# Kernel tuning notes

Hardware: AMD Instinct MI355X
Metric: run time of the kernel (lower is better)

Reference implementation:

```python
import jax, jax.numpy as jnp
import numpy as np

LN_EPS = 1e-5
NEG_INF = -1e30


def setup_inputs() -> dict:
    key = jax.random.key(0)
    ks = jax.random.split(key, 8)
    B, S, D_MODEL, Q_IN = 1, 2048, 1024, 512
    HI, DI = 16, 64            # indexer heads / head_dim
    H, DQK, DV = 8, 64, 64     # MLA heads, qk_head_dim, v_head_dim
    return {
        "x": jax.random.normal(ks[0], (B, S, D_MODEL), jnp.float32),
        "q_input": jax.random.normal(ks[1], (B, S, Q_IN), jnp.float32),
        "q": jax.random.normal(ks[2], (B, S, H, DQK), jnp.float32),
        "k": jax.random.normal(ks[3], (B, S, H, DQK), jnp.float32),
        "v": jax.random.normal(ks[4], (B, S, H, DV), jnp.float32),
        "w_q": jax.random.normal(ks[5], (Q_IN, HI * DI), jnp.float32) * (Q_IN ** -0.5),
        "w_k": jax.random.normal(ks[6], (D_MODEL, DI), jnp.float32) * (D_MODEL ** -0.5),
        "ln_g": jnp.ones((DI,), jnp.float32),
        "ln_b": jnp.zeros((DI,), jnp.float32),
        "w_weights": jax.random.normal(ks[7], (D_MODEL, HI), jnp.float32) * (D_MODEL ** -0.5),
        "top_k": 128,
    }


def _indexer_topk(x, q_input, w_q, w_k, ln_g, ln_b, w_weights, top_k):
    """Lightning indexer: per-head relevance scores -> weighted sum -> causal top-k indices."""
    B, S, _ = x.shape
    HI = w_weights.shape[1]
    DI = w_k.shape[1]
    qi = (q_input @ w_q).reshape(B, S, HI, DI)          # bqhd
    ki = x @ w_k                                         # bkd
    mu = ki.mean(-1, keepdims=True)
    var = ((ki - mu) ** 2).mean(-1, keepdims=True)
    ki = (ki - mu) * jax.lax.rsqrt(var + LN_EPS) * ln_g + ln_b
    # per-head weights; scores*w summed over h == (sum_h w*q) . k  (fused, same math)
    w = (x @ w_weights) * (HI ** -0.5)                   # bqh
    q_eff = jnp.einsum("bqhd,bqh->bqd", qi, w) * (DI ** -0.5)
    scores = jnp.einsum("bqd,bkd->bqk", q_eff, ki)       # [B,S,S]
    pos = jnp.arange(S)
    causal = jnp.where(pos[None, :] <= pos[:, None], 0.0, NEG_INF).astype(scores.dtype)
    scores = scores + causal[None]
    return jax.lax.top_k(scores, top_k)[1]               # [B,S,K]


def reference(x, q_input, q, k, v, w_q, w_k, ln_g, ln_b, w_weights, top_k):
    B, S, H, DQK = q.shape
    DV = v.shape[-1]
    idx = _indexer_topk(x, q_input, w_q, w_k, ln_g, ln_b, w_weights, top_k)  # [B,S,K]

    qh = q.transpose(0, 2, 1, 3)   # [B,H,Sq,D]
    kh = k.transpose(0, 2, 1, 3)   # [B,H,Sk,D]
    vh = v.transpose(0, 2, 1, 3)

    def gather(kv, ix):            # kv [Sk,D], ix [Sq,K] -> [Sq,K,D]
        return kv[ix]

    gather_h = jax.vmap(gather, in_axes=(0, None))       # over heads, shared idx
    gather_bh = jax.vmap(gather_h, in_axes=(0, 0))       # over batch
    k_sel = gather_bh(kh, idx)     # [B,H,Sq,K,D]
    v_sel = gather_bh(vh, idx)     # [B,H,Sq,K,Dv]

    att = jnp.einsum("bhqd,bhqkd->bhqk", qh, k_sel) * (DQK ** -0.5)
    pos = jnp.arange(S)
    valid = idx[:, None, :, :] <= pos[None, None, :, None]   # causal validity of gathered idx
    att = jnp.where(valid, att, NEG_INF)
    p = jax.nn.softmax(att, axis=-1)
    out = jnp.einsum("bhqk,bhqkd->bhqd", p, v_sel)
    return out.transpose(0, 2, 1, 3)   # [B,S,H,Dv]
```

## Files before the change

kernel.cpp:

```cpp
#include <hip/hip_runtime.h>
#include <hip/hip_bf16.h>
#include <hip/hip_fp16.h>
#include <math.h>

#define S 2048
#define DM 1024
#define QIN 512
#define HI 16
#define DI 64
#define NH 8
#define TOPK 128
#define LN_EPS 1e-5f
#define KP 8
#define KVSZ (S * NH * 64)

typedef float f32x4 __attribute__((ext_vector_type(4)));
typedef short s16x8 __attribute__((ext_vector_type(8)));

__device__ __forceinline__ float wave_sum(float v){
#pragma unroll
  for (int o = 32; o; o >>= 1) v += __shfl_xor(v, o);
  return v;
}
__device__ __forceinline__ float wave_max(float v){
#pragma unroll
  for (int o = 32; o; o >>= 1) v = fmaxf(v, __shfl_xor(v, o));
  return v;
}
__device__ __forceinline__ unsigned short f2bf(float x){
  unsigned u = __float_as_uint(x);
  unsigned r = u + 0x7FFFu + ((u >> 16) & 1u);
  return (unsigned short)(r >> 16);
}
__device__ __forceinline__ float bf2f(unsigned short s){
  return __uint_as_float(((unsigned)s) << 16);
}
__device__ __forceinline__ unsigned short f2h(float x){
  return __half_as_ushort(__float2half_rn(x));
}
union UH2 { unsigned int u; __half2 h; };
__device__ __forceinline__ __half2 as_half2(unsigned int u){ UH2 x; x.u = u; return x.h; }

#define MFMA3(ACC, AH, AL, BH, BL) \
  ACC = __builtin_amdgcn_mfma_f32_16x16x32_bf16(AH, BH, ACC, 0, 0, 0); \
  ACC = __builtin_amdgcn_mfma_f32_16x16x32_bf16(AH, BL, ACC, 0, 0, 0); \
  ACC = __builtin_amdgcn_mfma_f32_16x16x32_bf16(AL, BH, ACC, 0, 0, 0);

#define MFMA6(ACC, AH, AM, AL, BH, BM, BL) \
  ACC = __builtin_amdgcn_mfma_f32_16x16x32_bf16(AH, BH, ACC, 0, 0, 0); \
  ACC = __builtin_amdgcn_mfma_f32_16x16x32_bf16(AH, BM, ACC, 0, 0, 0); \
  ACC = __builtin_amdgcn_mfma_f32_16x16x32_bf16(AM, BH, ACC, 0, 0, 0); \
  ACC = __builtin_amdgcn_mfma_f32_16x16x32_bf16(AH, BL, ACC, 0, 0, 0); \
  ACC = __builtin_amdgcn_mfma_f32_16x16x32_bf16(AL, BH, ACC, 0, 0, 0); \
  ACC = __builtin_amdgcn_mfma_f32_16x16x32_bf16(AM, BM, ACC, 0, 0, 0);

__global__ __launch_bounds__(256) void k_f1(const float* __restrict__ x,
                                            const float* __restrict__ wk,
                                            const float* __restrict__ ww,
                                            float* __restrict__ part,
                                            const float* __restrict__ qin,
                                            unsigned short* __restrict__ Ah,
                                            unsigned short* __restrict__ Al,
                                            const float* __restrict__ k,
                                            unsigned short* __restrict__ kh,
                                            const float* __restrict__ v,
                                            unsigned short* __restrict__ vh,
                                            const float* __restrict__ wq,
                                            unsigned short* __restrict__ Bh,
                                            unsigned short* __restrict__ Bl){
  __shared__ float As[32][68];
  __shared__ float Bs[32][84];
  const int bid = blockIdx.x;
  const int t = threadIdx.x;

  if (bid < 256){
    const int kp = bid & 7;
    const int bm = bid >> 3;
    const int m0 = bm * 64;
    const int tm = (t & 15) * 4;
    const int tn = (t >> 4) * 5;
    float acc[4][5];
#pragma unroll
    for (int i = 0; i < 4; i++)
#pragma unroll
      for (int j = 0; j < 5; j++) acc[i][j] = 0.f;

    for (int kb = 0; kb < (DM / KP) / 32; ++kb){
      const int k0 = kp * (DM / KP) + kb * 32;
#pragma unroll
      for (int i = 0; i < 2; i++){
        int u = t + i * 256;
        int m = u >> 3, c4 = u & 7;
        float4 a = *(const float4*)&x[(size_t)(m0 + m) * DM + k0 + c4 * 4];
        As[c4*4+0][m] = a.x; As[c4*4+1][m] = a.y; As[c4*4+2][m] = a.z; As[c4*4+3][m] = a.w;
      }
#pragma unroll
      for (int i = 0; i < 10; i++){
        int u = t + i * 256;
        int kk = u / 80, nn = u % 80;
        float val = (nn < 64) ? wk[(size_t)(k0 + kk) * 64 + nn]
                              : ww[(size_t)(k0 + kk) * 16 + (nn - 64)];
        Bs[kk][nn] = val;
      }
      __syncthreads();
#pragma unroll
      for (int kk = 0; kk < 32; ++kk){
        float4 a = *(const float4*)&As[kk][tm];
        float av[4] = {a.x, a.y, a.z, a.w};
        float bb[5];
#pragma unroll
        for (int j = 0; j < 5; j++) bb[j] = Bs[kk][tn + j];
#pragma unroll
        for (int i = 0; i < 4; i++)
#pragma unroll
          for (int j = 0; j < 5; j++) acc[i][j] = fmaf(av[i], bb[j], acc[i][j]);
      }
      __syncthreads();
    }
    float* dst = part + (size_t)kp * S * 80;
#pragma unroll
    for (int i = 0; i < 4; i++)
#pragma unroll
      for (int j = 0; j < 5; j++)
        dst[(size_t)(m0 + tm + i) * 80 + tn + j] = acc[i][j];
    return;
  }

  if (bid < 256 + 3072){
    const int SEG0 = S * QIN / 4;
    const int SEG1 = KVSZ / 4;
    int id = (bid - 256) * 256 + t;
    if (id < SEG0){
      float4 f = ((const float4*)qin)[id];
      ushort4 h, lo;
      h.x = f2bf(f.x); lo.x = f2bf(f.x - bf2f(h.x));
      h.y = f2bf(f.y); lo.y = f2bf(f.y - bf2f(h.y));
      h.z = f2bf(f.z); lo.z = f2bf(f.z - bf2f(h.z));
      h.w = f2bf(f.w); lo.w = f2bf(f.w - bf2f(h.w));
      ((ushort4*)Ah)[id] = h;
      ((ushort4*)Al)[id] = lo;
    } else if (id < SEG0 + SEG1){
      int j = id - SEG0;
      float4 f = ((const float4*)k)[j];
      ushort4 o;
      o.x = f2h(f.x); o.y = f2h(f.y); o.z = f2h(f.z); o.w = f2h(f.w);
      ((ushort4*)kh)[j] = o;
    } else {
      int j = id - SEG0 - SEG1;
      float4 f = ((const float4*)v)[j];
      ushort4 o;
      o.x = f2h(f.x); o.y = f2h(f.y); o.z = f2h(f.z); o.w = f2h(f.w);
      ((ushort4*)vh)[j] = o;
    }
    return;
  }

  {
    unsigned short (*lh)[33] = (unsigned short(*)[33])&As[0][0];
    unsigned short (*ll)[33] = (unsigned short(*)[33])&Bs[0][0];
    const int b2 = bid - 3328;
    const int k0 = (b2 & 15) * 32;
    const int n0 = (b2 >> 4) * 32;
    const int c = t & 31, r8 = t >> 5;
#pragma unroll
    for (int i = 0; i < 4; ++i){
      int kk = r8 + i * 8;
      float wv = wq[(size_t)(k0 + kk) * 1024 + n0 + c];
      unsigned short h = f2bf(wv);
      lh[c][kk] = h;
      ll[c][kk] = f2bf(wv - bf2f(h));
    }
    __syncthreads();
    const int kk = t & 31, nl = t >> 5;
#pragma unroll
    for (int i = 0; i < 4; ++i){
      int nn = nl + i * 8;
      Bh[(size_t)(n0 + nn) * QIN + k0 + kk] = lh[nn][kk];
      Bl[(size_t)(n0 + nn) * QIN + k0 + kk] = ll[nn][kk];
    }
  }
}

__global__ __launch_bounds__(256) void k_f2(const float* __restrict__ part,
                                            const float* __restrict__ g,
                                            const float* __restrict__ b,
                                            unsigned short* __restrict__ kih,
                                            unsigned short* __restrict__ kim,
                                            unsigned short* __restrict__ kil,
                                            float* __restrict__ wgt,
                                            const unsigned short* __restrict__ Ah,
                                            const unsigned short* __restrict__ Al,
                                            const unsigned short* __restrict__ Bh,
                                            const unsigned short* __restrict__ Bl,
                                            float* __restrict__ qi){
  __shared__ short Ash[64][72];
  __shared__ short Asl[64][72];
  __shared__ short Bsh[64][72];
  __shared__ short Bsl[64][72];
  const int bid = blockIdx.x;
  const int t = threadIdx.x;
  if (bid < 512){
    const int s = bid * 4 + (t >> 6);
    const int l = t & 63;
    float kv = 0.f;
#pragma unroll
    for (int p = 0; p < KP; p++) kv += part[(size_t)p * S * 80 + (size_t)s * 80 + l];
    float wv = 0.f;
    if (l < 16){
#pragma unroll
      for (int p = 0; p < KP; p++) wv += part[(size_t)p * S * 80 + (size_t)s * 80 + 64 + l];
    }
    float mu = wave_sum(kv) * (1.f / 64.f);
    float d  = kv - mu;
    float var = wave_sum(d * d) * (1.f / 64.f);
    float o = d * (1.f / sqrtf(var + LN_EPS)) * g[l] + b[l];
    unsigned short h = f2bf(o);
    float r1 = o - bf2f(h);
    unsigned short m = f2bf(r1);
    kih[(size_t)s * 64 + l] = h;
    kim[(size_t)s * 64 + l] = m;
    kil[(size_t)s * 64 + l] = f2bf(r1 - bf2f(m));
    if (l < 16) wgt[(size_t)s * 16 + l] = wv * 0.25f;
    return;
  }
  const int b2 = bid - 512;
  const int bn = b2 & 15;
  const int bm = b2 >> 4;
  const int w = t >> 6, l = t & 63;
  const int r = l & 15, kg = l >> 4;
  const int m0 = bm * 64 + (w >> 1) * 32;
  const int n0 = bn * 64 + (w & 1) * 32;
  const int mq = (w >> 1) * 32;
  const int nq = (w & 1) * 32;
  const int srow = t >> 3;
  const int scol = (t & 7) * 8;

  f32x4 acc00 = {0,0,0,0}, acc01 = {0,0,0,0}, acc10 = {0,0,0,0}, acc11 = {0,0,0,0};

  for (int kb = 0; kb < QIN / 64; ++kb){
    const int k0 = kb * 64;
#pragma unroll
    for (int i = 0; i < 2; ++i){
      int row = srow + i * 32;
      size_t ga = (size_t)(bm * 64 + row) * QIN + k0 + scol;
      size_t gb = (size_t)(bn * 64 + row) * QIN + k0 + scol;
      *(s16x8*)&Ash[row][scol] = *(const s16x8*)(Ah + ga);
      *(s16x8*)&Asl[row][scol] = *(const s16x8*)(Al + ga);
      *(s16x8*)&Bsh[row][scol] = *(const s16x8*)(Bh + gb);
      *(s16x8*)&Bsl[row][scol] = *(const s16x8*)(Bl + gb);
    }
    __syncthreads();
#pragma unroll
    for (int ks = 0; ks < 2; ++ks){
      const int ko = ks * 32 + kg * 8;
      s16x8 ah0 = *(const s16x8*)&Ash[mq + r][ko];
      s16x8 ah1 = *(const s16x8*)&Ash[mq + 16 + r][ko];
      s16x8 al0 = *(const s16x8*)&Asl[mq + r][ko];
      s16x8 al1 = *(const s16x8*)&Asl[mq + 16 + r][ko];
      s16x8 bh0 = *(const s16x8*)&Bsh[nq + r][ko];
      s16x8 bh1 = *(const s16x8*)&Bsh[nq + 16 + r][ko];
      s16x8 bl0 = *(const s16x8*)&Bsl[nq + r][ko];
      s16x8 bl1 = *(const s16x8*)&Bsl[nq + 16 + r][ko];
      MFMA3(acc00, ah0, al0, bh0, bl0)
      MFMA3(acc01, ah0, al0, bh1, bl1)
      MFMA3(acc10, ah1, al1, bh0, bl0)
      MFMA3(acc11, ah1, al1, bh1, bl1)
    }
    __syncthreads();
  }
#pragma unroll
  for (int j = 0; j < 4; ++j){
    qi[(size_t)(m0 +  0 + kg * 4 + j) * 1024 + n0 +  0 + r] = acc00[j];
    qi[(size_t)(m0 +  0 + kg * 4 + j) * 1024 + n0 + 16 + r] = acc01[j];
    qi[(size_t)(m0 + 16 + kg * 4 + j) * 1024 + n0 +  0 + r] = acc10[j];
    qi[(size_t)(m0 + 16 + kg * 4 + j) * 1024 + n0 + 16 + r] = acc11[j];
  }
}

__global__ __launch_bounds__(256) void k_f3(const float* __restrict__ qi,
                                            const float* __restrict__ wgt,
                                            unsigned short* __restrict__ qeh,
                                            unsigned short* __restrict__ qem,
                                            unsigned short* __restrict__ qel){
  const int id = blockIdx.x * 256 + threadIdx.x;
  const int s = id >> 6, d = id & 63;
  float acc = 0.f;
#pragma unroll
  for (int h = 0; h < 16; h++)
    acc = fmaf(wgt[(size_t)s * 16 + h], qi[(size_t)s * 1024 + h * 64 + d], acc);
  acc *= 0.125f;
  unsigned short hh = f2bf(acc);
  float r1 = acc - bf2f(hh);
  unsigned short mm = f2bf(r1);
  qeh[(size_t)s * 64 + d] = hh;
  qem[(size_t)s * 64 + d] = mm;
  qel[(size_t)s * 64 + d] = f2bf(r1 - bf2f(mm));
}

__global__ __launch_bounds__(256) void k_scores(const unsigned short* __restrict__ qeh,
                                                const unsigned short* __restrict__ qem,
                                                const unsigned short* __restrict__ qel,
                                                const unsigned short* __restrict__ kih,
                                                const unsigned short* __restrict__ kim,
                                                const unsigned short* __restrict__ kil,
                                                float* __restrict__ sc){
  const int bj = blockIdx.x, bi = blockIdx.y;
  if (bj > bi) return;
  const int w = threadIdx.x >> 6, l = threadIdx.x & 63;
  const int r = l & 15, kg = l >> 4;
  const int m0 = bi * 64 + (w >> 1) * 32;
  const int n0 = bj * 64 + (w & 1) * 32;
  f32x4 acc00 = {0,0,0,0}, acc01 = {0,0,0,0}, acc10 = {0,0,0,0}, acc11 = {0,0,0,0};
  const size_t aoff = (size_t)(m0 + r) * 64 + kg * 8;
  const size_t boff = (size_t)(n0 + r) * 64 + kg * 8;
#pragma unroll
  for (int k0 = 0; k0 < 64; k0 += 32){
    s16x8 ah0 = *(const s16x8*)(qeh + aoff + k0);
    s16x8 ah1 = *(const s16x8*)(qeh + aoff + 16 * 64 + k0);
    s16x8 am0 = *(const s16x8*)(qem + aoff + k0);
    s16x8 am1 = *(const s16x8*)(qem + aoff + 16 * 64 + k0);
    s16x8 al0 = *(const s16x8*)(qel + aoff + k0);
    s16x8 al1 = *(const s16x8*)(qel + aoff + 16 * 64 + k0);
    s16x8 bh0 = *(const s16x8*)(kih + boff + k0);
    s16x8 bh1 = *(const s16x8*)(kih + boff + 16 * 64 + k0);
    s16x8 bm0 = *(const s16x8*)(kim + boff + k0);
    s16x8 bm1 = *(const s16x8*)(kim + boff + 16 * 64 + k0);
    s16x8 bl0 = *(const s16x8*)(kil + boff + k0);
    s16x8 bl1 = *(const s16x8*)(kil + boff + 16 * 64 + k0);
    MFMA6(acc00, ah0, am0, al0, bh0, bm0, bl0)
    MFMA6(acc01, ah0, am0, al0, bh1, bm1, bl1)
    MFMA6(acc10, ah1, am1, al1, bh0, bm0, bl0)
    MFMA6(acc11, ah1, am1, al1, bh1, bm1, bl1)
  }
#pragma unroll
  for (int j = 0; j < 4; ++j){
    sc[(size_t)(m0 +  0 + kg * 4 + j) * S + n0 +  0 + r] = acc00[j];
    sc[(size_t)(m0 +  0 + kg * 4 + j) * S + n0 + 16 + r] = acc01[j];
    sc[(size_t)(m0 + 16 + kg * 4 + j) * S + n0 +  0 + r] = acc10[j];
    sc[(size_t)(m0 + 16 + kg * 4 + j) * S + n0 + 16 + r] = acc11[j];
  }
}

__global__ __launch_bounds__(256) void k_topk(const float* __restrict__ sc,
                                              int* __restrict__ idx,
                                              int* __restrict__ cnt){
  const int i = blockIdx.x, t = threadIdx.x;
  const int w = t >> 6, l = t & 63;
  const int n = i + 1;
  int* outr = idx + (size_t)i * TOPK;
  if (n <= TOPK){
    for (int m = t; m < n; m += 256) outr[m] = m;
    if (t == 0) cnt[i] = n;
    return;
  }
  __shared__ unsigned int keys[S];
  __shared__ int lA[S];
  __shared__ int lB[S];
  __shared__ int hist[256];
  __shared__ int wtot[4];
  __shared__ int s_b, s_above, s_out, s_m;
  hist[t] = 0;
  if (t == 0) s_out = 0;
  __syncthreads();
  for (int j = t; j < n; j += 256){
    unsigned int u = __float_as_uint(sc[(size_t)i * S + j]);
    unsigned int kk = (u & 0x80000000u) ? ~u : (u | 0x80000000u);
    keys[j] = kk;
    atomicAdd(&hist[kk >> 24], 1);
  }
  __syncthreads();
  int rem = TOPK;
  {
    const int h = hist[t];
    int vsc = h;
#pragma unroll
    for (int off = 1; off < 64; off <<= 1){
      int u = __shfl_down(vsc, off);
      if (l + off < 64) vsc += u;
    }
    if (l == 0) wtot[w] = vsc;
    __syncthreads();
    int later = 0;
#pragma unroll
    for (int ww = 1; ww < 4; ++ww) if (ww > w) later += wtot[ww];
    const int excl = vsc + later - h;
    if (excl < rem && excl + h >= rem){ s_b = t; s_above = excl; }
    __syncthreads();
  }
  int b = s_b;
  rem -= s_above;
  if (t == 0) s_m = 0;
  __syncthreads();
  for (int j = t; j < n; j += 256){
    int by = keys[j] >> 24;
    if (by > b){ int p = atomicAdd(&s_out, 1); outr[p] = j; }
    else if (by == b){ int p = atomicAdd(&s_m, 1); lA[p] = j; }
  }
  __syncthreads();
  int m = s_m;
  int* Lsrc = lA; int* Ldst = lB;
  bool done = false;
  if (m == rem){
    int base = TOPK - rem;
    for (int u = t; u < m; u += 256) outr[base + u] = Lsrc[u];
    done = true;
  }
  for (int p = 2; p >= 0 && !done; --p){
    const int sh = p * 8;
    __syncthreads();
    hist[t] = 0;
    __syncthreads();
    for (int u = t; u < m; u += 256) atomicAdd(&hist[(keys[Lsrc[u]] >> sh) & 255], 1);
    __syncthreads();
    {
      const int h = hist[t];
      int vsc = h;
#pragma unroll
      for (int off = 1; off < 64; off <<= 1){
        int u = __shfl_down(vsc, off);
        if (l + off < 64) vsc += u;
      }
      if (l == 0) wtot[w] = vsc;
      __syncthreads();
      int later = 0;
#pragma unroll
      for (int ww = 1; ww < 4; ++ww) if (ww > w) later += wtot[ww];
      const int excl = vsc + later - h;
      if (excl < rem && excl + h >= rem){ s_b = t; s_above = excl; }
      __syncthreads();
    }
    b = s_b;
    rem -= s_above;
    if (t == 0) s_m = 0;
    __syncthreads();
    for (int u = t; u < m; u += 256){
      int j = Lsrc[u]; int by = (keys[j] >> sh) & 255;
      if (by > b){ int p2 = atomicAdd(&s_out, 1); outr[p2] = j; }
      else if (by == b){ int p2 = atomicAdd(&s_m, 1); Ldst[p2] = j; }
    }
    __syncthreads();
    m = s_m;
    { int* tmp = Lsrc; Lsrc = Ldst; Ldst = tmp; }
    if (m == rem){
      int base = TOPK - rem;
      for (int u = t; u < m; u += 256) outr[base + u] = Lsrc[u];
      done = true;
    }
  }
  if (!done && t == 0){
    int base = TOPK - rem;
    for (int a = 0; a < rem; ++a){
      int mn = 1 << 30, pos = -1;
      for (int u = 0; u < m; ++u){ int j = Lsrc[u]; if (j < mn){ mn = j; pos = u; } }
      outr[base + a] = mn; Lsrc[pos] = 1 << 30;
    }
  }
  if (t == 0) cnt[i] = TOPK;
}

__global__ __launch_bounds__(256) void k_attn(const float* __restrict__ q,
                                              const unsigned short* __restrict__ kh,
                                              const unsigned short* __restrict__ vh,
                                              const int* __restrict__ idx,
                                              const int* __restrict__ cnt,
                                              float* __restrict__ out){
  const int i = blockIdx.x;
  const int w = threadIdx.x >> 6, l = threadIdx.x & 63;
  const int n = cnt[i];
  const int* irow = idx + (size_t)i * TOPK;

  __shared__ int   sidx[4][TOPK];
  __shared__ float sp[4][2][TOPK];

  sidx[w][l]      = (l < n)      ? irow[l]      : 0;
  sidx[w][l + 64] = (l + 64 < n) ? irow[l + 64] : 0;

  const int h0 = 2 * w, h1 = h0 + 1;
  const int g = l >> 3, gl = l & 7;
  const float* qrow = q + (size_t)i * (NH * 64);
  __half2 qa2[4], qb2[4];
  {
    float4 a0 = *(const float4*)&qrow[h0 * 64 + gl * 8];
    float4 a1 = *(const float4*)&qrow[h0 * 64 + gl * 8 + 4];
    float4 b0 = *(const float4*)&qrow[h1 * 64 + gl * 8];
    float4 b1 = *(const float4*)&qrow[h1 * 64 + gl * 8 + 4];
    qa2[0] = __floats2half2_rn(a0.x * 0.125f, a0.y * 0.125f);
    qa2[1] = __floats2half2_rn(a0.z * 0.125f, a0.w * 0.125f);
    qa2[2] = __floats2half2_rn(a1.x * 0.125f, a1.y * 0.125f);
    qa2[3] = __floats2half2_rn(a1.z * 0.125f, a1.w * 0.125f);
    qb2[0] = __floats2half2_rn(b0.x * 0.125f, b0.y * 0.125f);
    qb2[1] = __floats2half2_rn(b0.z * 0.125f, b0.w * 0.125f);
    qb2[2] = __floats2half2_rn(b1.x * 0.125f, b1.y * 0.125f);
    qb2[3] = __floats2half2_rn(b1.z * 0.125f, b1.w * 0.125f);
  }
  asm volatile("" ::: "memory");

#pragma unroll 4
  for (int pass = 0; pass < TOPK / 8; ++pass){
    const int j = pass * 8 + g;
    const size_t base = (size_t)sidx[w][j] * (NH * 64);
    uint4 u0 = *(const uint4*)(kh + base + h0 * 64 + gl * 8);
    uint4 u1 = *(const uint4*)(kh + base + h1 * 64 + gl * 8);
    __half2 acc0 = __floats2half2_rn(0.f, 0.f);
    __half2 acc1 = __floats2half2_rn(0.f, 0.f);
    acc0 = __hfma2(as_half2(u0.x), qa2[0], acc0);
    acc0 = __hfma2(as_half2(u0.y), qa2[1], acc0);
    acc0 = __hfma2(as_half2(u0.z), qa2[2], acc0);
    acc0 = __hfma2(as_half2(u0.w), qa2[3], acc0);
    acc1 = __hfma2(as_half2(u1.x), qb2[0], acc1);
    acc1 = __hfma2(as_half2(u1.y), qb2[1], acc1);
    acc1 = __hfma2(as_half2(u1.z), qb2[2], acc1);
    acc1 = __hfma2(as_half2(u1.w), qb2[3], acc1);
    float d0 = __low2float(acc0) + __high2float(acc0);
    float d1 = __low2float(acc1) + __high2float(acc1);
#pragma unroll
    for (int o = 1; o < 8; o <<= 1){ d0 += __shfl_xor(d0, o); d1 += __shfl_xor(d1, o); }
    if (gl == 0){ sp[w][0][j] = d0; sp[w][1][j] = d1; }
  }
  asm volatile("" ::: "memory");

  const bool v0 = (l < n), v1 = (l + 64 < n);
  {
    float s0 = v0 ? sp[w][0][l] : -1e30f, s1 = v1 ? sp[w][0][l + 64] : -1e30f;
    float m = wave_max(fmaxf(s0, s1));
    float e0 = v0 ? __expf(s0 - m) : 0.f;
    float e1 = v1 ? __expf(s1 - m) : 0.f;
    float inv = 1.f / wave_sum(e0 + e1);
    sp[w][0][l] = e0 * inv;
    sp[w][0][l + 64] = e1 * inv;
  }
  {
    float s0 = v0 ? sp[w][1][l] : -1e30f, s1 = v1 ? sp[w][1][l + 64] : -1e30f;
    float m = wave_max(fmaxf(s0, s1));
    float e0 = v0 ? __expf(s0 - m) : 0.f;
    float e1 = v1 ? __expf(s1 - m) : 0.f;
    float inv = 1.f / wave_sum(e0 + e1);
    sp[w][1][l] = e0 * inv;
    sp[w][1][l + 64] = e1 * inv;
  }
  asm volatile("" ::: "memory");

  const int kq = l >> 4;
  const int hp = (l >> 3) & 1;
  const int d8 = (l & 7) * 8;
  float o8[8] = {0,0,0,0,0,0,0,0};
#pragma unroll 4
  for (int pass = 0; pass < TOPK / 4; ++pass){
    const int j = pass * 4 + kq;
    const size_t base = (size_t)sidx[w][j] * (NH * 64);
    uint4 uv = *(const uint4*)(vh + base + (h0 + hp) * 64 + d8);
    float p = sp[w][hp][j];
    __half2 va = as_half2(uv.x), vb = as_half2(uv.y), vc = as_half2(uv.z), vd = as_half2(uv.w);
    o8[0] = fmaf(p, __low2float(va),  o8[0]);
    o8[1] = fmaf(p, __high2float(va), o8[1]);
    o8[2] = fmaf(p, __low2float(vb),  o8[2]);
    o8[3] = fmaf(p, __high2float(vb), o8[3]);
    o8[4] = fmaf(p, __low2float(vc),  o8[4]);
    o8[5] = fmaf(p, __high2float(vc), o8[5]);
    o8[6] = fmaf(p, __low2float(vd),  o8[6]);
    o8[7] = fmaf(p, __high2float(vd), o8[7]);
  }
#pragma unroll
  for (int e = 0; e < 8; ++e){
    o8[e] += __shfl_xor(o8[e], 16);
    o8[e] += __shfl_xor(o8[e], 32);
  }
  if (l < 16){
    float* dst = &out[(size_t)i * (NH * 64) + (h0 + hp) * 64 + d8];
    *(float4*)dst       = make_float4(o8[0], o8[1], o8[2], o8[3]);
    *(float4*)(dst + 4) = make_float4(o8[4], o8[5], o8[6], o8[7]);
  }
}

extern "C" void kernel_launch(void* const* d_in, const int* in_sizes, int n_in,
                              void* d_out, int out_size, void* d_ws, size_t ws_size,
                              hipStream_t stream){
  const float* x   = (const float*)d_in[0];
  const float* qin = (const float*)d_in[1];
  const float* q   = (const float*)d_in[2];
  const float* k   = (const float*)d_in[3];
  const float* v   = (const float*)d_in[4];
  const float* wq  = (const float*)d_in[5];
  const float* wk  = (const float*)d_in[6];
  const float* lng = (const float*)d_in[7];
  const float* lnb = (const float*)d_in[8];
  const float* ww  = (const float*)d_in[9];
  float* out = (float*)d_out;

  float* ws = (float*)d_ws;
  float* part = ws;
  float* wgt  = ws + 1310720;
  float* qi   = ws + 1343488;
  float* sc   = ws + 3440640;
  int*   idx  = (int*)(ws + 7634944);
  int*   cnt  = (int*)(ws + 7897088);
  unsigned short* kh  = (unsigned short*)(ws + 7899136);
  unsigned short* vh  = (unsigned short*)(ws + 8423424);
  unsigned short* kih = (unsigned short*)(ws + 8947712);
  unsigned short* kim = (unsigned short*)(ws + 9013248);
  unsigned short* kil = (unsigned short*)(ws + 9078784);
  unsigned short* qeh = (unsigned short*)(ws + 9144320);
  unsigned short* qem = (unsigned short*)(ws + 9209856);
  unsigned short* qel = (unsigned short*)(ws + 9275392);
  unsigned short* Ah  = (unsigned short*)(ws + 9340928);
  unsigned short* Al  = (unsigned short*)(ws + 9865216);
  unsigned short* Bh  = (unsigned short*)(ws + 10389504);
  unsigned short* Bl  = (unsigned short*)(ws + 10651648);

  hipLaunchKernelGGL(k_f1,     dim3(3840),   dim3(256), 0, stream,
                     x, wk, ww, part, qin, Ah, Al, k, kh, v, vh, wq, Bh, Bl);
  hipLaunchKernelGGL(k_f2,     dim3(1024),   dim3(256), 0, stream,
                     part, lng, lnb, kih, kim, kil, wgt, Ah, Al, Bh, Bl, qi);
  hipLaunchKernelGGL(k_f3,     dim3(512),    dim3(256), 0, stream,
                     qi, wgt, qeh, qem, qel);
  hipLaunchKernelGGL(k_scores, dim3(32, 32), dim3(256), 0, stream,
                     qeh, qem, qel, kih, kim, kil, sc);
  hipLaunchKernelGGL(k_topk,   dim3(2048),   dim3(256), 0, stream, sc, idx, cnt);
  hipLaunchKernelGGL(k_attn,   dim3(2048),   dim3(256), 0, stream, q, kh, vh, idx, cnt, out);
}
```

Measured before the change: 97.88 us.

## Fuse top-k selection into sparse attention kernel and double split-K partitions

```diff
diff --git a/kernel.cpp b/kernel.cpp
--- a/kernel.cpp
+++ b/kernel.cpp
@@ -11,7 +11,7 @@
 #define NH 8
 #define TOPK 128
 #define LN_EPS 1e-5f
-#define KP 8
+#define KP 16
 #define KVSZ (S * NH * 64)
 
 typedef float f32x4 __attribute__((ext_vector_type(4)));
@@ -73,9 +73,9 @@
   const int bid = blockIdx.x;
   const int t = threadIdx.x;
 
-  if (bid < 256){
-    const int kp = bid & 7;
-    const int bm = bid >> 3;
+  if (bid < 512){
+    const int kp = bid & 15;
+    const int bm = bid >> 4;
     const int m0 = bm * 64;
     const int tm = (t & 15) * 4;
     const int tn = (t >> 4) * 5;
@@ -126,10 +126,10 @@
     return;
   }
 
-  if (bid < 256 + 3072){
+  if (bid < 512 + 3072){
     const int SEG0 = S * QIN / 4;
     const int SEG1 = KVSZ / 4;
-    int id = (bid - 256) * 256 + t;
+    int id = (bid - 512) * 256 + t;
     if (id < SEG0){
       float4 f = ((const float4*)qin)[id];
       ushort4 h, lo;
@@ -158,7 +158,7 @@
   {
     unsigned short (*lh)[33] = (unsigned short(*)[33])&As[0][0];
     unsigned short (*ll)[33] = (unsigned short(*)[33])&Bs[0][0];
-    const int b2 = bid - 3328;
+    const int b2 = bid - 3584;
     const int k0 = (b2 & 15) * 32;
     const int n0 = (b2 >> 4) * 32;
     const int c = t & 31, r8 = t >> 5;
@@ -341,77 +341,39 @@
   }
 }
 
-__global__ __launch_bounds__(256) void k_topk(const float* __restrict__ sc,
-                                              int* __restrict__ idx,
-                                              int* __restrict__ cnt){
+__global__ __launch_bounds__(256) void k_ta(const float* __restrict__ sc,
+                                            const float* __restrict__ q,
+                                            const unsigned short* __restrict__ kh,
+                                            const unsigned short* __restrict__ vh,
+                                            float* __restrict__ out){
   const int i = blockIdx.x, t = threadIdx.x;
   const int w = t >> 6, l = t & 63;
-  const int n = i + 1;
-  int* outr = idx + (size_t)i * TOPK;
-  if (n <= TOPK){
-    for (int m = t; m < n; m += 256) outr[m] = m;
-    if (t == 0) cnt[i] = n;
-    return;
-  }
+  const int ncand = i + 1;
+
   __shared__ unsigned int keys[S];
   __shared__ int lA[S];
   __shared__ int lB[S];
   __shared__ int hist[256];
   __shared__ int wtot[4];
+  __shared__ int sres[TOPK];
   __shared__ int s_b, s_above, s_out, s_m;
-  hist[t] = 0;
-  if (t == 0) s_out = 0;
-  __syncthreads();
-  for (int j = t; j < n; j += 256){
-    unsigned int u = __float_as_uint(sc[(size_t)i * S + j]);
-    unsigned int kk = (u & 0x80000000u) ? ~u : (u | 0x80000000u);
-    keys[j] = kk;
-    atomicAdd(&hist[kk >> 24], 1);
-  }
-  __syncthreads();
-  int rem = TOPK;
-  {
-    const int h = hist[t];
-    int vsc = h;
-#pragma unroll
-    for (int off = 1; off < 64; off <<= 1){
-      int u = __shfl_down(vsc, off);
-      if (l + off < 64) vsc += u;
-    }
-    if (l == 0) wtot[w] = vsc;
-    __syncthreads();
-    int later = 0;
-#pragma unroll
-    for (int ww = 1; ww < 4; ++ww) if (ww > w) later += wtot[ww];
-    const int excl = vsc + later - h;
-    if (excl < rem && excl + h >= rem){ s_b = t; s_above = excl; }
-    __syncthreads();
-  }
-  int b = s_b;
-  rem -= s_above;
-  if (t == 0) s_m = 0;
-  __syncthreads();
-  for (int j = t; j < n; j += 256){
-    int by = keys[j] >> 24;
-    if (by > b){ int p = atomicAdd(&s_out, 1); outr[p] = j; }
-    else if (by == b){ int p = atomicAdd(&s_m, 1); lA[p] = j; }
-  }
-  __syncthreads();
-  int m = s_m;
-  int* Lsrc = lA; int* Ldst = lB;
-  bool done = false;
-  if (m == rem){
-    int base = TOPK - rem;
-    for (int u = t; u < m; u += 256) outr[base + u] = Lsrc[u];
-    done = true;
-  }
-  for (int p = 2; p >= 0 && !done; --p){
-    const int sh = p * 8;
-    __syncthreads();
+  __shared__ float sp[4][2][TOPK];
+
+  if (ncand <= TOPK){
+    if (t < TOPK) sres[t] = (t < ncand) ? t : 0;
+    __syncthreads();
+  } else {
     hist[t] = 0;
-    __syncthreads();
-    for (int u = t; u < m; u += 256) atomicAdd(&hist[(keys[Lsrc[u]] >> sh) & 255], 1);
-    __syncthreads();
+    if (t == 0) s_out = 0;
+    __syncthreads();
+    for (int j = t; j < ncand; j += 256){
+      unsigned int u = __float_as_uint(sc[(size_t)i * S + j]);
+      unsigned int kk = (u & 0x80000000u) ? ~u : (u | 0x80000000u);
+      keys[j] = kk;
+      atomicAdd(&hist[kk >> 24], 1);
+    }
+    __syncthreads();
+    int rem = TOPK;
     {
       const int h = hist[t];
       int vsc = h;
@@ -429,52 +391,93 @@
       if (excl < rem && excl + h >= rem){ s_b = t; s_above = excl; }
       __syncthreads();
     }
-    b = s_b;
+    int b = s_b;
     rem -= s_above;
     if (t == 0) s_m = 0;
     __syncthreads();
-    for (int u = t; u < m; u += 256){
-      int j = Lsrc[u]; int by = (keys[j] >> sh) & 255;
-      if (by > b){ int p2 = atomicAdd(&s_out, 1); outr[p2] = j; }
-      else if (by == b){ int p2 = atomicAdd(&s_m, 1); Ldst[p2] = j; }
-    }
-    __syncthreads();
-    m = s_m;
-    { int* tmp = Lsrc; Lsrc = Ldst; Ldst = tmp; }
+    for (int b0 = 0; b0 < ncand; b0 += 256){
+      int j = b0 + t;
+      bool valid = j < ncand;
+      unsigned int kk = valid ? keys[j] : 0u;
+      int by = kk >> 24;
+      bool pgt = valid && (by > b);
+      bool peq = valid && (by == b);
+      unsigned long long mgt = __ballot(pgt);
+      unsigned long long meq = __ballot(peq);
+      int basegt = 0, baseeq = 0;
+      if (l == 0){
+        basegt = atomicAdd(&s_out, __popcll(mgt));
+        baseeq = atomicAdd(&s_m, __popcll(meq));
+      }
+      basegt = __shfl(basegt, 0);
+      baseeq = __shfl(baseeq, 0);
+      unsigned long long lanemask = (1ull << l) - 1ull;
+      if (pgt) sres[basegt + __popcll(mgt & lanemask)] = j;
+      if (peq) lA[baseeq + __popcll(meq & lanemask)] = j;
+    }
+    __syncthreads();
+    int m = s_m;
+    int* Lsrc = lA; int* Ldst = lB;
+    bool done = false;
     if (m == rem){
       int base = TOPK - rem;
-      for (int u = t; u < m; u += 256) outr[base + u] = Lsrc[u];
+      for (int u = t; u < m; u += 256) sres[base + u] = Lsrc[u];
       done = true;
     }
-  }
-  if (!done && t == 0){
-    int base = TOPK - rem;
-    for (int a = 0; a < rem; ++a){
-      int mn = 1 << 30, pos = -1;
-      for (int u = 0; u < m; ++u){ int j = Lsrc[u]; if (j < mn){ mn = j; pos = u; } }
-      outr[base + a] = mn; Lsrc[pos] = 1 << 30;
-    }
-  }
-  if (t == 0) cnt[i] = TOPK;
-}
-
-__global__ __launch_bounds__(256) void k_attn(const float* __restrict__ q,
-                                              const unsigned short* __restrict__ kh,
-                                              const unsigned short* __restrict__ vh,
-                                              const int* __restrict__ idx,
-                                              const int* __restrict__ cnt,
-                                              float* __restrict__ out){
-  const int i = blockIdx.x;
-  const int w = threadIdx.x >> 6, l = threadIdx.x & 63;
-  const int n = cnt[i];
-  const int* irow = idx + (size_t)i * TOPK;
-
-  __shared__ int   sidx[4][TOPK];
-  __shared__ float sp[4][2][TOPK];
-
-  sidx[w][l]      = (l < n)      ? irow[l]      : 0;
-  sidx[w][l + 64] = (l + 64 < n) ? irow[l + 64] : 0;
-
+    for (int p = 2; p >= 0 && !done; --p){
+      const int sh = p * 8;
+      __syncthreads();
+      hist[t] = 0;
+      __syncthreads();
+      for (int u = t; u < m; u += 256) atomicAdd(&hist[(keys[Lsrc[u]] >> sh) & 255], 1);
+      __syncthreads();
+      {
+        const int h = hist[t];
+        int vsc = h;
+#pragma unroll
+        for (int off = 1; off < 64; off <<= 1){
+          int u = __shfl_down(vsc, off);
+          if (l + off < 64) vsc += u;
+        }
+        if (l == 0) wtot[w] = vsc;
+        __syncthreads();
+        int later = 0;
+#pragma unroll
+        for (int ww = 1; ww < 4; ++ww) if (ww > w) later += wtot[ww];
+        const int excl = vsc + later - h;
+        if (excl < rem && excl + h >= rem){ s_b = t; s_above = excl; }
+        __syncthreads();
+      }
+      b = s_b;
+      rem -= s_above;
+      if (t == 0) s_m = 0;
+      __syncthreads();
+      for (int u = t; u < m; u += 256){
+        int j = Lsrc[u]; int by = (keys[j] >> sh) & 255;
+        if (by > b){ int p2 = atomicAdd(&s_out, 1); sres[p2] = j; }
+        else if (by == b){ int p2 = atomicAdd(&s_m, 1); Ldst[p2] = j; }
+      }
+      __syncthreads();
+      m = s_m;
+      { int* tmp = Lsrc; Lsrc = Ldst; Ldst = tmp; }
+      if (m == rem){
+        int base = TOPK - rem;
+        for (int u = t; u < m; u += 256) sres[base + u] = Lsrc[u];
+        done = true;
+      }
+    }
+    if (!done && t == 0){
+      int base = TOPK - rem;
+      for (int a = 0; a < rem; ++a){
+        int mn = 1 << 30, pos = -1;
+        for (int u = 0; u < m; ++u){ int j = Lsrc[u]; if (j < mn){ mn = j; pos = u; } }
+        sres[base + a] = mn; Lsrc[pos] = 1 << 30;
+      }
+    }
+    __syncthreads();
+  }
+
+  const int n = (ncand < TOPK) ? ncand : TOPK;
   const int h0 = 2 * w, h1 = h0 + 1;
   const int g = l >> 3, gl = l & 7;
   const float* qrow = q + (size_t)i * (NH * 64);
@@ -493,12 +496,12 @@
     qb2[2] = __floats2half2_rn(b1.x * 0.125f, b1.y * 0.125f);
     qb2[3] = __floats2half2_rn(b1.z * 0.125f, b1.w * 0.125f);
   }
-  asm volatile("" ::: "memory");
-
-#pragma unroll 4
+
+#pragma unroll 8
   for (int pass = 0; pass < TOPK / 8; ++pass){
     const int j = pass * 8 + g;
-    const size_t base = (size_t)sidx[w][j] * (NH * 64);
+    const int sj = (j < n) ? sres[j] : 0;
+    const size_t base = (size_t)sj * (NH * 64);
     uint4 u0 = *(const uint4*)(kh + base + h0 * 64 + gl * 8);
     uint4 u1 = *(const uint4*)(kh + base + h1 * 64 + gl * 8);
     __half2 acc0 = __floats2half2_rn(0.f, 0.f);
@@ -544,10 +547,11 @@
   const int hp = (l >> 3) & 1;
   const int d8 = (l & 7) * 8;
   float o8[8] = {0,0,0,0,0,0,0,0};
-#pragma unroll 4
+#pragma unroll 8
   for (int pass = 0; pass < TOPK / 4; ++pass){
     const int j = pass * 4 + kq;
-    const size_t base = (size_t)sidx[w][j] * (NH * 64);
+    const int sj = (j < n) ? sres[j] : 0;
+    const size_t base = (size_t)sj * (NH * 64);
     uint4 uv = *(const uint4*)(vh + base + (h0 + hp) * 64 + d8);
     float p = sp[w][hp][j];
     __half2 va = as_half2(uv.x), vb = as_half2(uv.y), vc = as_half2(uv.z), vd = as_half2(uv.w);
@@ -589,25 +593,23 @@
 
   float* ws = (float*)d_ws;
   float* part = ws;
-  float* wgt  = ws + 1310720;
-  float* qi   = ws + 1343488;
-  float* sc   = ws + 3440640;
-  int*   idx  = (int*)(ws + 7634944);
-  int*   cnt  = (int*)(ws + 7897088);
-  unsigned short* kh  = (unsigned short*)(ws + 7899136);
-  unsigned short* vh  = (unsigned short*)(ws + 8423424);
-  unsigned short* kih = (unsigned short*)(ws + 8947712);
-  unsigned short* kim = (unsigned short*)(ws + 9013248);
-  unsigned short* kil = (unsigned short*)(ws + 9078784);
-  unsigned short* qeh = (unsigned short*)(ws + 9144320);
-  unsigned short* qem = (unsigned short*)(ws + 9209856);
-  unsigned short* qel = (unsigned short*)(ws + 9275392);
-  unsigned short* Ah  = (unsigned short*)(ws + 9340928);
-  unsigned short* Al  = (unsigned short*)(ws + 9865216);
-  unsigned short* Bh  = (unsigned short*)(ws + 10389504);
-  unsigned short* Bl  = (unsigned short*)(ws + 10651648);
-
-  hipLaunchKernelGGL(k_f1,     dim3(3840),   dim3(256), 0, stream,
+  float* wgt  = ws + 2621440;
+  float* qi   = ws + 2654208;
+  float* sc   = ws + 4751360;
+  unsigned short* kh  = (unsigned short*)(ws + 8945664);
+  unsigned short* vh  = (unsigned short*)(ws + 9469952);
+  unsigned short* kih = (unsigned short*)(ws + 9994240);
+  unsigned short* kim = (unsigned short*)(ws + 10059776);
+  unsigned short* kil = (unsigned short*)(ws + 10125312);
+  unsigned short* qeh = (unsigned short*)(ws + 10190848);
+  unsigned short* qem = (unsigned short*)(ws + 10256384);
+  unsigned short* qel = (unsigned short*)(ws + 10321920);
+  unsigned short* Ah  = (unsigned short*)(ws + 10387456);
+  unsigned short* Al  = (unsigned short*)(ws + 10911744);
+  unsigned short* Bh  = (unsigned short*)(ws + 11436032);
+  unsigned short* Bl  = (unsigned short*)(ws + 11698176);
+
+  hipLaunchKernelGGL(k_f1,     dim3(4096),   dim3(256), 0, stream,
                      x, wk, ww, part, qin, Ah, Al, k, kh, v, vh, wq, Bh, Bl);
   hipLaunchKernelGGL(k_f2,     dim3(1024),   dim3(256), 0, stream,
                      part, lng, lnb, kih, kim, kil, wgt, Ah, Al, Bh, Bl, qi);
@@ -615,6 +617,6 @@
                      qi, wgt, qeh, qem, qel);
   hipLaunchKernelGGL(k_scores, dim3(32, 32), dim3(256), 0, stream,
                      qeh, qem, qel, kih, kim, kil, sc);
-  hipLaunchKernelGGL(k_topk,   dim3(2048),   dim3(256), 0, stream, sc, idx, cnt);
-  hipLaunchKernelGGL(k_attn,   dim3(2048),   dim3(256), 0, stream, q, kh, vh, idx, cnt, out);
-}
+  hipLaunchKernelGGL(k_ta,     dim3(2048),   dim3(256), 0, stream,
+                     sc, q, kh, vh, out);
+}
```

After: 98.95 us. No clear change (+1.1%).
